# Performance work log

Hardware: AMD Instinct MI355X
Metric: run time of the kernel (lower is better)

## Reference

```python
import jax, jax.numpy as jnp
import numpy as np

NODES = 163842
IN_FEATS = 32
OUT_FEATS = 64

def setup_inputs() -> dict:
    key = jax.random.key(0)
    k1, k2, k3, k4, k5 = jax.random.split(key, 5)
    x = jax.random.normal(k1, (NODES, IN_FEATS), dtype=jnp.float32)
    # 0-based neighbor indices (original stores 1-based and subtracts 1)
    neigh_indices = jax.random.randint(k2, (NODES, 25, 3), 0, NODES, dtype=jnp.int32)
    # barycentric interpolation weights per (node, 25 template positions, 3 triangle verts)
    neigh_weights = jax.random.uniform(k3, (NODES, 25, 3), dtype=jnp.float32)
    W = jax.random.normal(k4, (OUT_FEATS, 25 * IN_FEATS), dtype=jnp.float32) * 0.02
    b = jax.random.normal(k5, (OUT_FEATS,), dtype=jnp.float32) * 0.02
    return {"x": x, "neigh_indices": neigh_indices, "neigh_weights": neigh_weights, "W": W, "b": b}

def reference(x, neigh_indices, neigh_weights, W, b):
    nodes, c = x.shape
    # gather neighbor features: (nodes, 25, 3, in_feats)
    mat = x[neigh_indices.reshape(-1)].reshape(nodes, 25, 3, c)
    # barycentric weighted sum over the 3 triangle vertices -> (nodes, 25, in_feats)
    feat = jnp.sum(mat * neigh_weights[..., None], axis=2)
    # flatten the 25 template positions and project: (nodes, out_feats)
    feat = feat.reshape(nodes, 25 * c)
    return feat @ W.T + b
```

## Files before the change

### kernel.cpp

```cpp
#include <hip/hip_runtime.h>
#include <hip/hip_bf16.h>

#define NNODES   163842
#define INF      32
#define OUTF     64
#define NPOS     25
#define KTOT     800
#define MT       128
#define NTHREADS 512
#define NWAVES   8

typedef float    f32x4 __attribute__((ext_vector_type(4)));
typedef _Float16 f16x8 __attribute__((ext_vector_type(8)));

typedef const __attribute__((address_space(1))) void GV;
typedef __attribute__((address_space(3))) void LV;

__global__ void cvt_kernel(const float* __restrict__ x, const float* __restrict__ W,
                           _Float16* __restrict__ xh, _Float16* __restrict__ wh) {
    int tid = blockIdx.x * blockDim.x + threadIdx.x;
    int stride = gridDim.x * blockDim.x;
    const int nx8 = NNODES * INF / 8;
    const f32x4* x4 = (const f32x4*)x;
    f16x8* xh8 = (f16x8*)xh;
    for (int j = tid; j < nx8; j += stride) {
        f32x4 a = x4[2*j], b = x4[2*j+1];
        f16x8 o;
        #pragma unroll
        for (int k = 0; k < 4; ++k) { o[k] = (_Float16)a[k]; o[4+k] = (_Float16)b[k]; }
        xh8[j] = o;
    }
    f16x8* wh8 = (f16x8*)wh;
    for (int t = tid; t < NPOS * 4 * 64; t += stride) {
        const int l  = t & 63;
        const int nb = (t >> 6) & 3;
        const int p  = t >> 8;
        const int row = 16*nb + (l & 15);
        const int kb  = p*32 + (l >> 4)*8;
        const float* src = W + row * KTOT + kb;
        f16x8 o;
        #pragma unroll
        for (int j = 0; j < 8; ++j) o[j] = (_Float16)src[j];
        wh8[t] = o;
    }
}

__launch_bounds__(NTHREADS, 2)
__global__ void conv_mfma(const int* __restrict__ nidx, const float* __restrict__ nwt,
                          const _Float16* __restrict__ xh, const _Float16* __restrict__ wh,
                          const float* __restrict__ bias, float* __restrict__ out) {
    __shared__ __align__(16) _Float16 whl[NPOS * 4 * 64 * 8];
    __shared__ int      idxs[MT * 75];
    __shared__ _Float16 wtsl[MT * 75];

    const int tid  = threadIdx.x;
    const int blk  = blockIdx.x;
    const int lane = tid & 63;
    const int wave = tid >> 6;

    for (int i = wave; i < NPOS * 4; i += NWAVES) {
        __builtin_amdgcn_global_load_lds((GV*)((const char*)wh + i * 1024 + lane * 16),
                                         (LV*)((char*)whl + i * 1024), 16, 0, 0);
    }
    {
        const long gbase = (long)blk * (MT * 75);
        const long tot   = (long)NNODES * 75;
        for (int i = tid; i < MT * 75; i += NTHREADS) {
            long g = gbase + i;
            bool ok = g < tot;
            idxs[i] = ok ? nidx[g] : 0;
            wtsl[i] = ok ? (_Float16)nwt[g] : (_Float16)0.0f;
        }
    }

    const int arow  = lane & 15;
    const int kgrp  = lane >> 4;
    const int irow  = (wave * 16 + arow) * 75;
    const int node0 = blk * MT + wave * 16;
    const _Float16* xg = xh + kgrp * 8;

    __syncthreads();

    f32x4 acc0 = {0,0,0,0}, acc1 = {0,0,0,0}, acc2 = {0,0,0,0}, acc3 = {0,0,0,0};
    f16x8 g00, g01, g02, g10, g11, g12, g20, g21, g22, g30, g31, g32;

#define ISSUE(P, S) do {                                                        \
        const int _p = (P);                                                     \
        const int _i0 = idxs[irow + _p*3 + 0];                                  \
        const int _i1 = idxs[irow + _p*3 + 1];                                  \
        const int _i2 = idxs[irow + _p*3 + 2];                                  \
        const _Float16* _a0 = xg + (long)_i0 * INF;                             \
        const _Float16* _a1 = xg + (long)_i1 * INF;                             \
        const _Float16* _a2 = xg + (long)_i2 * INF;                             \
        asm volatile("global_load_dwordx4 %0, %1, off" : "=&v"(g##S##0) : "v"(_a0)); \
        asm volatile("global_load_dwordx4 %0, %1, off" : "=&v"(g##S##1) : "v"(_a1)); \
        asm volatile("global_load_dwordx4 %0, %1, off" : "=&v"(g##S##2) : "v"(_a2)); \
    } while (0)

#define STEP(P, S, VM, PI) do {                                                 \
        const int _p = (P);                                                     \
        const f16x8* _bwp = (const f16x8*)whl + _p * 256 + lane;                \
        const f16x8 _b0 = _bwp[0];                                              \
        const f16x8 _b1 = _bwp[64];                                             \
        const f16x8 _b2 = _bwp[128];                                            \
        const f16x8 _b3 = _bwp[192];                                            \
        const _Float16 _w0 = wtsl[irow + _p*3 + 0];                             \
        const _Float16 _w1 = wtsl[irow + _p*3 + 1];                             \
        const _Float16 _w2 = wtsl[irow + _p*3 + 2];                             \
        asm volatile("s_waitcnt vmcnt(" #VM ")" ::: "memory");                  \
        __builtin_amdgcn_sched_barrier(0);                                      \
        const f16x8 _af = g##S##0 * _w0 + g##S##1 * _w1 + g##S##2 * _w2;        \
        acc0 = __builtin_amdgcn_mfma_f32_16x16x32_f16(_b0, _af, acc0, 0, 0, 0); \
        acc1 = __builtin_amdgcn_mfma_f32_16x16x32_f16(_b1, _af, acc1, 0, 0, 0); \
        acc2 = __builtin_amdgcn_mfma_f32_16x16x32_f16(_b2, _af, acc2, 0, 0, 0); \
        acc3 = __builtin_amdgcn_mfma_f32_16x16x32_f16(_b3, _af, acc3, 0, 0, 0); \
        __builtin_amdgcn_sched_barrier(0);                                      \
        if ((PI) >= 0) ISSUE((PI), S);                                          \
        __builtin_amdgcn_sched_barrier(0);                                      \
    } while (0)

    ISSUE(0, 0); ISSUE(1, 1); ISSUE(2, 2); ISSUE(3, 3);

    for (int pp = 0; pp < 20; pp += 4) {
        STEP(pp + 0, 0, 9, pp + 4);
        STEP(pp + 1, 1, 9, pp + 5);
        STEP(pp + 2, 2, 9, pp + 6);
        STEP(pp + 3, 3, 9, pp + 7);
    }
    STEP(20, 0, 9, 24);
    STEP(21, 1, 9, -1);
    STEP(22, 2, 6, -1);
    STEP(23, 3, 3, -1);
    STEP(24, 0, 0, -1);

#undef ISSUE
#undef STEP

    const int node = node0 + arow;
    if (node < NNODES) {
        #pragma unroll
        for (int nb = 0; nb < 4; ++nb) {
            const int cb = 16*nb + 4*kgrp;
            const f32x4 b4 = *(const f32x4*)(bias + cb);
            f32x4 o;
            #pragma unroll
            for (int r = 0; r < 4; ++r) o[r] = (nb == 0 ? acc0 : nb == 1 ? acc1 : nb == 2 ? acc2 : acc3)[r] + b4[r];
            *(f32x4*)(out + (long)node * OUTF + cb) = o;
        }
    }
}

__global__ void conv_fallback(const float* __restrict__ x, const int* __restrict__ nidx,
                              const float* __restrict__ nwt, const float* __restrict__ W,
                              const float* __restrict__ bias, float* __restrict__ out) {
    __shared__ float feat[KTOT];
    const int n = blockIdx.x;
    const int t = threadIdx.x;
    for (int e = t; e < KTOT; e += 64) {
        const int p = e >> 5, c = e & 31;
        const int ib = n * 75 + p * 3;
        float a = 0.0f;
        #pragma unroll
        for (int v = 0; v < 3; ++v)
            a += nwt[ib+v] * x[nidx[ib+v] * INF + c];
        feat[e] = a;
    }
    __syncthreads();
    float a = bias[t];
    const float* wr = W + t * KTOT;
    for (int k = 0; k < KTOT; ++k) a += feat[k] * wr[k];
    out[(long)n * OUTF + t] = a;
}

extern "C" void kernel_launch(void* const* d_in, const int* in_sizes, int n_in,
                              void* d_out, int out_size, void* d_ws, size_t ws_size,
                              hipStream_t stream) {
    const float* x    = (const float*)d_in[0];
    const int*   nidx = (const int*)  d_in[1];
    const float* nwt  = (const float*)d_in[2];
    const float* W    = (const float*)d_in[3];
    const float* bias = (const float*)d_in[4];
    float* out = (float*)d_out;

    const size_t need = (size_t)NNODES * INF * 2 + (size_t)NPOS * 4 * 64 * 8 * 2;
    if (ws_size < need) {
        conv_fallback<<<NNODES, 64, 0, stream>>>(x, nidx, nwt, W, bias, out);
        return;
    }

    _Float16* xh = (_Float16*)d_ws;
    _Float16* wh = xh + (size_t)NNODES * INF;

    cvt_kernel<<<1024, 256, 0, stream>>>(x, W, xh, wh);
    const int nblocks = (NNODES + MT - 1) / MT;
    conv_mfma<<<nblocks, NTHREADS, 0, stream>>>(nidx, nwt, xh, wh, bias, out);
}
```

Before: 187.9 us.

## Split gather into three passes over source-node windows for cache locality

Runs the conv kernel three times, each pass gathering only neighbors whose index falls in a third of the node range (about 3.5 MB of fp16 features). Out-of-window indices are redirected to the window base with zero weight, and passes after the first accumulate into the output instead of adding bias. The goal is to keep the random gather's working set resident in L2/cache. The cost is three times the index/weight loading, LDS staging and MFMA work, plus extra output read-modify-write. Launch bounds are also relaxed to one block per SM.

New measurement: 309.7 us. 1.65x slower.

```diff
diff --git a/kernel.cpp b/kernel.cpp
--- a/kernel.cpp
+++ b/kernel.cpp
@@ -9,6 +9,7 @@
 #define MT       128
 #define NTHREADS 512
 #define NWAVES   8
+#define WSZ      54614
 
 typedef float    f32x4 __attribute__((ext_vector_type(4)));
 typedef _Float16 f16x8 __attribute__((ext_vector_type(8)));
@@ -45,10 +46,11 @@
     }
 }
 
-__launch_bounds__(NTHREADS, 2)
+__launch_bounds__(NTHREADS, 1)
 __global__ void conv_mfma(const int* __restrict__ nidx, const float* __restrict__ nwt,
                           const _Float16* __restrict__ xh, const _Float16* __restrict__ wh,
-                          const float* __restrict__ bias, float* __restrict__ out) {
+                          const float* __restrict__ bias, float* __restrict__ out,
+                          int lo, int phase) {
     __shared__ __align__(16) _Float16 whl[NPOS * 4 * 64 * 8];
     __shared__ int      idxs[MT * 75];
     __shared__ _Float16 wtsl[MT * 75];
@@ -86,9 +88,12 @@
 
 #define ISSUE(P, S) do {                                                        \
         const int _p = (P);                                                     \
-        const int _i0 = idxs[irow + _p*3 + 0];                                  \
-        const int _i1 = idxs[irow + _p*3 + 1];                                  \
-        const int _i2 = idxs[irow + _p*3 + 2];                                  \
+        int _i0 = idxs[irow + _p*3 + 0];                                        \
+        int _i1 = idxs[irow + _p*3 + 1];                                        \
+        int _i2 = idxs[irow + _p*3 + 2];                                        \
+        _i0 = ((unsigned)(_i0 - lo) < (unsigned)WSZ) ? _i0 : lo;                \
+        _i1 = ((unsigned)(_i1 - lo) < (unsigned)WSZ) ? _i1 : lo;                \
+        _i2 = ((unsigned)(_i2 - lo) < (unsigned)WSZ) ? _i2 : lo;                \
         const _Float16* _a0 = xg + (long)_i0 * INF;                             \
         const _Float16* _a1 = xg + (long)_i1 * INF;                             \
         const _Float16* _a2 = xg + (long)_i2 * INF;                             \
@@ -104,9 +109,13 @@
         const f16x8 _b1 = _bwp[64];                                             \
         const f16x8 _b2 = _bwp[128];                                            \
         const f16x8 _b3 = _bwp[192];                                            \
-        const _Float16 _w0 = wtsl[irow + _p*3 + 0];                             \
-        const _Float16 _w1 = wtsl[irow + _p*3 + 1];                             \
-        const _Float16 _w2 = wtsl[irow + _p*3 + 2];                             \
+        const int _j0 = idxs[irow + _p*3 + 0];                                  \
+        const int _j1 = idxs[irow + _p*3 + 1];                                  \
+        const int _j2 = idxs[irow + _p*3 + 2];                                  \
+        const _Float16 _z = (_Float16)0.0f;                                     \
+        const _Float16 _w0 = ((unsigned)(_j0 - lo) < (unsigned)WSZ) ? wtsl[irow + _p*3 + 0] : _z; \
+        const _Float16 _w1 = ((unsigned)(_j1 - lo) < (unsigned)WSZ) ? wtsl[irow + _p*3 + 1] : _z; \
+        const _Float16 _w2 = ((unsigned)(_j2 - lo) < (unsigned)WSZ) ? wtsl[irow + _p*3 + 2] : _z; \
         asm volatile("s_waitcnt vmcnt(" #VM ")" ::: "memory");                  \
         __builtin_amdgcn_sched_barrier(0);                                      \
         const f16x8 _af = g##S##0 * _w0 + g##S##1 * _w1 + g##S##2 * _w2;        \
@@ -141,11 +150,15 @@
         #pragma unroll
         for (int nb = 0; nb < 4; ++nb) {
             const int cb = 16*nb + 4*kgrp;
-            const f32x4 b4 = *(const f32x4*)(bias + cb);
+            float* dst = out + (long)node * OUTF + cb;
+            const f32x4 a = (nb == 0 ? acc0 : nb == 1 ? acc1 : nb == 2 ? acc2 : acc3);
+            f32x4 base4;
+            if (phase == 0) base4 = *(const f32x4*)(bias + cb);
+            else            base4 = *(const f32x4*)dst;
             f32x4 o;
             #pragma unroll
-            for (int r = 0; r < 4; ++r) o[r] = (nb == 0 ? acc0 : nb == 1 ? acc1 : nb == 2 ? acc2 : acc3)[r] + b4[r];
-            *(f32x4*)(out + (long)node * OUTF + cb) = o;
+            for (int r = 0; r < 4; ++r) o[r] = a[r] + base4[r];
+            *(f32x4*)dst = o;
         }
     }
 }
@@ -193,5 +206,7 @@
 
     cvt_kernel<<<1024, 256, 0, stream>>>(x, W, xh, wh);
     const int nblocks = (NNODES + MT - 1) / MT;
-    conv_mfma<<<nblocks, NTHREADS, 0, stream>>>(nidx, nwt, xh, wh, bias, out);
-}
+    conv_mfma<<<nblocks, NTHREADS, 0, stream>>>(nidx, nwt, xh, wh, bias, out, 0,       0);
+    conv_mfma<<<nblocks, NTHREADS, 0, stream>>>(nidx, nwt, xh, wh, bias, out, WSZ,     1);
+    conv_mfma<<<nblocks, NTHREADS, 0, stream>>>(nidx, nwt, xh, wh, bias, out, 2 * WSZ, 2);
+}
```
